# Kernel tuning notes

Measured on AMD Instinct MI355X. Metric: run time of the kernel, lower is better.

Reference implementation:

```python
import jax, jax.numpy as jnp
import numpy as np

H = 16  # n_heads
LN_EPS = 1e-5

def _ln(x, g, b):
    m = jnp.mean(x, axis=-1, keepdims=True)
    v = jnp.mean(jnp.square(x - m), axis=-1, keepdims=True)
    return (x - m) * jax.lax.rsqrt(v + LN_EPS) * g + b

def setup_inputs() -> dict:
    key = jax.random.key(0)
    ks = jax.random.split(key, 12)
    Nq, Nk, D = 4096, 4096, 1024
    s = 1.0 / np.sqrt(D)
    return {
        "query": jax.random.normal(ks[0], (Nq, D), jnp.float32),
        "key_": jax.random.normal(ks[1], (Nk, D), jnp.float32),
        "Wq": jax.random.uniform(ks[2], (D, D), jnp.float32, -s, s),
        "bq": jax.random.uniform(ks[3], (D,), jnp.float32, -s, s),
        "Wk": jax.random.uniform(ks[4], (D, D), jnp.float32, -s, s),
        "bk": jax.random.uniform(ks[5], (D,), jnp.float32, -s, s),
        "Wv": jax.random.uniform(ks[6], (D, D), jnp.float32, -s, s),
        "bv": jax.random.uniform(ks[7], (D,), jnp.float32, -s, s),
        "g1": jnp.ones((D,), jnp.float32),
        "b1": jnp.zeros((D,), jnp.float32),
        "Wl": jax.random.uniform(ks[8], (D, D), jnp.float32, -s, s),
        "bl": jax.random.uniform(ks[9], (D,), jnp.float32, -s, s),
        "g2": jnp.ones((D,), jnp.float32),
        "b2": jnp.zeros((D,), jnp.float32),
    }

def reference(query, key_, Wq, bq, Wk, bk, Wv, bv, g1, b1, Wl, bl, g2, b2):
    Nq, D = query.shape
    Nk = key_.shape[0]
    dh = D // H
    scale = 1.0 / jnp.sqrt(jnp.asarray(D, query.dtype))  # NOTE: full dim_V, not per-head
    Q = (query @ Wq + bq).reshape(Nq, H, dh)   # [Nq,H,dh]
    K = (key_ @ Wk + bk).reshape(Nk, H, dh)    # [Nk,H,dh]
    V = (key_ @ Wv + bv).reshape(Nk, H, dh)    # [Nk,H,dh]
    A = jax.nn.softmax(jnp.einsum('qhd,khd->hqk', Q, K) * scale, axis=-1)  # [H,Nq,Nk]
    O = Q + jnp.einsum('hqk,khd->qhd', A, V)   # residual on projected Q
    out = _ln(O.reshape(Nq, D), g1, b1)
    out = out + jax.nn.relu(out @ Wl + bl)
    return _ln(out, g2, b2)
```

## Files before the change

kernel.cpp:

```cpp
#include <hip/hip_runtime.h>
#include <hip/hip_bf16.h>
#include <stdint.h>

typedef __attribute__((ext_vector_type(4))) float  f32x4;
typedef __attribute__((ext_vector_type(8))) short  bf16x8;
typedef __attribute__((ext_vector_type(4))) float  float4v;
typedef __attribute__((ext_vector_type(4))) unsigned short u16x4;
typedef __attribute__((ext_vector_type(4))) uint32_t u32x4;

typedef uint32_t u32_as1 __attribute__((address_space(1)));
typedef uint32_t u32_as3 __attribute__((address_space(3)));

#define CEXP_SCALE 0.045084221f
#define INV_CEXP   22.180710f

__device__ __forceinline__ void gload_lds16(const void* g, void* l) {
  __builtin_amdgcn_global_load_lds((const u32_as1*)g, (u32_as3*)l, 16, 0, 0);
}

__device__ __forceinline__ unsigned short f2bf(float f) {
  union { float f; uint32_t u; } v; v.f = f;
  uint32_t r = v.u + 0x7fffu + ((v.u >> 16) & 1u);
  return (unsigned short)(r >> 16);
}
__device__ __forceinline__ float bf2f(unsigned short u) {
  union { uint32_t u; float f; } v; v.u = ((uint32_t)u) << 16;
  return v.f;
}
__device__ __forceinline__ uint32_t cvtpk_bf16(float lo, float hi) {
  uint32_t d;
  asm("v_cvt_pk_bf16_f32 %0, %1, %2" : "=v"(d) : "v"(lo), "v"(hi));
  return d;
}
__device__ __forceinline__ float exp2_hw(float x) {
  float r;
  asm("v_exp_f32 %0, %1" : "=v"(r) : "v"(x));
  return r;
}

__global__ __launch_bounds__(256) void wtrans4(const float* __restrict__ W0,
                                               const float* __restrict__ W1,
                                               const float* __restrict__ W2,
                                               const float* __restrict__ W3,
                                               unsigned short* __restrict__ WT, int D) {
  __shared__ float tile[32][33];
  const float* W = (blockIdx.z == 0) ? W0 : (blockIdx.z == 1) ? W1 : (blockIdx.z == 2) ? W2 : W3;
  unsigned short* WTz = WT + (size_t)blockIdx.z * D * D;
  int r0 = blockIdx.x * 32;
  int c0 = blockIdx.y * 32;
  int tc = threadIdx.x & 31;
  int tr = (threadIdx.x >> 5) * 4;
#pragma unroll
  for (int i = 0; i < 4; i++)
    tile[tr + i][tc] = W[(size_t)(r0 + tr + i) * D + c0 + tc];
  __syncthreads();
#pragma unroll
  for (int i = 0; i < 4; i++)
    WTz[(size_t)(c0 + tr + i) * D + r0 + tc] = f2bf(tile[tc][tr + i]);
}

template <int AF32>
__device__ __forceinline__ void gemm_core(
    const void* __restrict__ Ain, const unsigned short* __restrict__ BT,
    const float* __restrict__ bias, const float* __restrict__ bias2,
    unsigned short* __restrict__ C, unsigned short* __restrict__ VtOut,
    const unsigned short* __restrict__ RES,
    int M, int K, int relu_res, float cscale, int bm, int bn,
    unsigned char* AsmRaw, unsigned short* Bsm) {
  int tid = threadIdx.x;
  int lane = tid & 63;
  int w = tid >> 6;
  int wr = (w >> 1) * 64;
  int wc = (w & 1) * 64;
  int r = lane & 15;
  int q4 = lane >> 4;

  f32x4 acc[4][4] = {};

  for (int k0 = 0; k0 < K; k0 += 64) {
    if (AF32) {
      const float* Af = (const float*)Ain;
#pragma unroll
      for (int i = 0; i < 8; i++) {
        int idx = i * 256 + tid;
        int row = idx >> 4;
        int cg = (idx & 15) ^ (row & 15);
        gload_lds16(Af + (size_t)(bm + row) * K + k0 + cg * 4,
                    (float*)AsmRaw + idx * 4);
      }
    } else {
      const unsigned short* Ab = (const unsigned short*)Ain;
#pragma unroll
      for (int i = 0; i < 4; i++) {
        int idx = i * 256 + tid;
        int row = idx >> 3;
        int g = ((idx & 7) ^ (row & 7)) * 8;
        gload_lds16(Ab + (size_t)(bm + row) * K + k0 + g,
                    (unsigned short*)AsmRaw + idx * 8);
      }
    }
#pragma unroll
    for (int i = 0; i < 4; i++) {
      int idx = i * 256 + tid;
      int row = idx >> 3;
      int g = ((idx & 7) ^ (row & 7)) * 8;
      gload_lds16(BT + (size_t)(bn + row) * K + k0 + g, &Bsm[idx * 8]);
    }
    __syncthreads();
#pragma unroll
    for (int kk = 0; kk < 2; kk++) {
      bf16x8 af[4], bfr[4];
      if (AF32) {
        const float* AsF = (const float*)AsmRaw;
        int c0 = kk * 8 + q4 * 2;
#pragma unroll
        for (int mb = 0; mb < 4; mb++) {
          int row = wr + mb * 16 + r;
          const float* rp = AsF + row * 64;
          int x = row & 15;
          f32x4 a0 = *(const f32x4*)(rp + ((c0 ^ x) * 4));
          f32x4 a1 = *(const f32x4*)(rp + (((c0 + 1) ^ x) * 4));
          u32x4 t = {cvtpk_bf16(a0.x, a0.y), cvtpk_bf16(a0.z, a0.w),
                     cvtpk_bf16(a1.x, a1.y), cvtpk_bf16(a1.z, a1.w)};
          af[mb] = __builtin_bit_cast(bf16x8, t);
        }
      } else {
        const unsigned short* AsB = (const unsigned short*)AsmRaw;
        int ch = ((kk * 4 + q4) ^ (r & 7)) * 8;
#pragma unroll
        for (int mb = 0; mb < 4; mb++)
          af[mb] = *(const bf16x8*)&AsB[(wr + mb * 16 + r) * 64 + ch];
      }
      int chb = ((kk * 4 + q4) ^ (r & 7)) * 8;
#pragma unroll
      for (int nb = 0; nb < 4; nb++)
        bfr[nb] = *(const bf16x8*)&Bsm[(wc + nb * 16 + r) * 64 + chb];
#pragma unroll
      for (int mb = 0; mb < 4; mb++)
#pragma unroll
        for (int nb = 0; nb < 4; nb++)
          acc[mb][nb] = __builtin_amdgcn_mfma_f32_16x16x32_bf16(af[mb], bfr[nb], acc[mb][nb], 0, 0, 0);
    }
    __syncthreads();
  }

#pragma unroll
  for (int mb = 0; mb < 4; mb++) {
#pragma unroll
    for (int nb = 0; nb < 4; nb++) {
      int col = bn + wc + nb * 16 + r;
      bool second = (VtOut != nullptr) && (col >= 1024);
      int ccol = second ? (col - 1024) : col;
      float bv = second ? bias2[ccol] : bias[ccol];
      if (second) {
        u16x4 ov;
#pragma unroll
        for (int rr = 0; rr < 4; rr++)
          ov[rr] = f2bf(acc[mb][nb][rr] + bv);
        int row0 = bm + wr + mb * 16 + q4 * 4;
        *(u16x4*)(VtOut + (size_t)ccol * M + row0) = ov;
      } else {
#pragma unroll
        for (int rr = 0; rr < 4; rr++) {
          int row = bm + wr + mb * 16 + q4 * 4 + rr;
          float v = acc[mb][nb][rr] + bv;
          if (relu_res) {
            float res = bf2f(RES[(size_t)row * 1024 + ccol]);
            v = res + (v > 0.f ? v : 0.f);
          }
          C[(size_t)row * 1024 + ccol] = f2bf(v * cscale);
        }
      }
    }
  }
}

__global__ __launch_bounds__(256) void proj_gemm(
    const float* __restrict__ query, const float* __restrict__ key_,
    const unsigned short* __restrict__ WqT, const unsigned short* __restrict__ WkvT,
    const float* __restrict__ bq, const float* __restrict__ bk, const float* __restrict__ bv,
    unsigned short* __restrict__ Qs, unsigned short* __restrict__ Kp,
    unsigned short* __restrict__ Vt, int Nq, int D) {
  __shared__ __align__(16) unsigned char AsmRaw[128 * 64 * 4];
  __shared__ __align__(16) unsigned short Bsm[128 * 64];
  int bid = blockIdx.x;
  if (bid < 256) {
    gemm_core<1>(query, WqT, bq, nullptr, Qs, nullptr, nullptr,
                 Nq, D, 0, CEXP_SCALE, (bid & 31) * 128, (bid >> 5) * 128, AsmRaw, Bsm);
  } else {
    int b = bid - 256;
    gemm_core<1>(key_, WkvT, bk, bv, Kp, Vt, nullptr,
                 Nq, D, 0, 1.0f, (b & 31) * 128, (b >> 5) * 128, AsmRaw, Bsm);
  }
}

__global__ __launch_bounds__(256) void ffn_gemm(
    const unsigned short* __restrict__ A, const unsigned short* __restrict__ WlT,
    const float* __restrict__ bl, unsigned short* __restrict__ C,
    const unsigned short* __restrict__ RES, int Nq, int D) {
  __shared__ __align__(16) unsigned short Asm[2][128 * 64];
  __shared__ __align__(16) unsigned short Bsm[2][128 * 64];
  int tid = threadIdx.x;
  int lane = tid & 63;
  int w = tid >> 6;
  int wr = (w >> 1) * 64;
  int wc = (w & 1) * 64;
  int bid = blockIdx.x;
  int bm = (bid & 31) * 128;
  int bn = (bid >> 5) * 128;
  int r = lane & 15;
  int q4 = lane >> 4;

  f32x4 acc[4][4] = {};

  auto STAGE = [&](int nb, int k0) {
#pragma unroll
    for (int i = 0; i < 4; i++) {
      int idx = i * 256 + tid;
      int row = idx >> 3;
      int g = ((idx & 7) ^ (row & 7)) * 8;
      gload_lds16(A + (size_t)(bm + row) * D + k0 + g, &Asm[nb][idx * 8]);
      gload_lds16(WlT + (size_t)(bn + row) * D + k0 + g, &Bsm[nb][idx * 8]);
    }
  };

  STAGE(0, 0);
  __syncthreads();

  int cur = 0;
  const int NT = D >> 6;
  for (int t = 0; t < NT; ++t) {
    if (t + 1 < NT) STAGE(cur ^ 1, (t + 1) * 64);
#pragma unroll
    for (int kk = 0; kk < 2; kk++) {
      int ch = ((kk * 4 + q4) ^ (r & 7)) * 8;
      bf16x8 af[4], bfr[4];
#pragma unroll
      for (int mb = 0; mb < 4; mb++)
        af[mb] = *(const bf16x8*)&Asm[cur][(wr + mb * 16 + r) * 64 + ch];
#pragma unroll
      for (int nb = 0; nb < 4; nb++)
        bfr[nb] = *(const bf16x8*)&Bsm[cur][(wc + nb * 16 + r) * 64 + ch];
#pragma unroll
      for (int mb = 0; mb < 4; mb++)
#pragma unroll
        for (int nb = 0; nb < 4; nb++)
          acc[mb][nb] = __builtin_amdgcn_mfma_f32_16x16x32_bf16(af[mb], bfr[nb], acc[mb][nb], 0, 0, 0);
    }
    __syncthreads();
    cur ^= 1;
  }

#pragma unroll
  for (int mb = 0; mb < 4; mb++) {
#pragma unroll
    for (int nb = 0; nb < 4; nb++) {
      int col = bn + wc + nb * 16 + r;
      float bv = bl[col];
#pragma unroll
      for (int rr = 0; rr < 4; rr++) {
        int row = bm + wr + mb * 16 + q4 * 4 + rr;
        float v = acc[mb][nb][rr] + bv;
        float res = bf2f(RES[(size_t)row * 1024 + col]);
        v = res + (v > 0.f ? v : 0.f);
        C[(size_t)row * 1024 + col] = f2bf(v);
      }
    }
  }
}

__global__ __launch_bounds__(256, 4) void attn_kernel(
    const unsigned short* __restrict__ Qs,
    const unsigned short* __restrict__ Kp,
    const unsigned short* __restrict__ Vt,
    unsigned short* __restrict__ Opart,
    float* __restrict__ Lpart,
    int Nq, int Nk) {
  __shared__ __align__(16) unsigned short Ksm[2][4096];
  __shared__ __align__(16) unsigned short Vsm[2][4096];
  const int Dm = 1024;
  int tid = threadIdx.x;
  int w = tid >> 6;
  int lane = tid & 63;
  int r = lane & 15;
  int q4 = lane >> 4;
  int bid = blockIdx.x;
  int vid = ((bid & 7) << 7) + (bid >> 3);
  int h = vid >> 6;
  int qw = ((vid >> 1) & 31) * 128 + w * 32;
  int z = vid & 1;
  int k_beg = z * (Nk >> 1);
  const int NT = Nk >> 7;

  const unsigned short* Kb = Kp + h * 64;
  const unsigned short* Vb = Vt + (size_t)h * 64 * Nk;

  int srcA = r + ((lane & 16) << 1);
  int srcB = srcA + 16;
  bool hi_cb = (lane & 32) != 0;

  bf16x8 qf[2][2];
#pragma unroll
  for (int mb = 0; mb < 2; mb++)
#pragma unroll
    for (int s = 0; s < 2; s++)
      qf[mb][s] = *(const bf16x8*)(Qs + (size_t)(qw + mb * 16 + r) * Dm + h * 64 + s * 32 + q4 * 8);

  bf16x8 ones;
#pragma unroll
  for (int i = 0; i < 8; i++) ones[i] = (short)0x3F80;

  const f32x4 czero = {0.f, 0.f, 0.f, 0.f};
  f32x4 acc[2][4] = {};
  f32x4 acc_s[2] = {};

  auto STAGE = [&](int nb, int key0) {
    if (w < 2) {
#pragma unroll
      for (int k = 0; k < 4; k++) {
        int j = w * 4 + k;
        int s = j >> 2, cb = j & 3;
        gload_lds16(Kb + (size_t)(key0 + cb * 16 + r) * Dm + s * 32 + q4 * 8,
                    &Ksm[nb][j * 512]);
      }
    } else {
#pragma unroll
      for (int k = 0; k < 4; k++) {
        int j = (w - 2) * 4 + k;
        int s = j >> 2, db = j & 3;
        gload_lds16(Vb + (size_t)(db * 16 + r) * Nk + key0 + s * 32 + q4 * 8,
                    &Vsm[nb][j * 512]);
      }
    }
  };

  STAGE(0, k_beg);
  __syncthreads();

  int cur = 0;
  for (int t = 0; t < NT; ++t) {
    if (t + 1 < NT) STAGE(cur ^ 1, k_beg + (t + 1) * 64);

    bf16x8 kfr0[4], kfr1[4];
#pragma unroll
    for (int cb = 0; cb < 4; cb++) {
      kfr0[cb] = *(const bf16x8*)&Ksm[cur][(0 * 4 + cb) * 512 + lane * 8];
      kfr1[cb] = *(const bf16x8*)&Ksm[cur][(1 * 4 + cb) * 512 + lane * 8];
    }
    f32x4 sacc[2][4];
#pragma unroll
    for (int cb = 0; cb < 4; cb++)
#pragma unroll
      for (int mb = 0; mb < 2; mb++)
        sacc[mb][cb] = __builtin_amdgcn_mfma_f32_16x16x32_bf16(kfr0[cb], qf[mb][0], czero, 0, 0, 0);
#pragma unroll
    for (int cb = 0; cb < 4; cb++)
#pragma unroll
      for (int mb = 0; mb < 2; mb++)
        sacc[mb][cb] = __builtin_amdgcn_mfma_f32_16x16x32_bf16(kfr1[cb], qf[mb][1], sacc[mb][cb], 0, 0, 0);

    uint32_t pk[2][4][2];
#pragma unroll
    for (int mb = 0; mb < 2; mb++)
#pragma unroll
      for (int cb = 0; cb < 4; cb++) {
        float p0 = exp2_hw(sacc[mb][cb][0]);
        float p1 = exp2_hw(sacc[mb][cb][1]);
        float p2 = exp2_hw(sacc[mb][cb][2]);
        float p3 = exp2_hw(sacc[mb][cb][3]);
        pk[mb][cb][0] = cvtpk_bf16(p0, p1);
        pk[mb][cb][1] = cvtpk_bf16(p2, p3);
      }

#pragma unroll
    for (int s = 0; s < 2; s++) {
      bf16x8 pf[2];
#pragma unroll
      for (int mb = 0; mb < 2; mb++) {
        uint32_t s0 = hi_cb ? pk[mb][2 * s + 1][0] : pk[mb][2 * s][0];
        uint32_t s1 = hi_cb ? pk[mb][2 * s + 1][1] : pk[mb][2 * s][1];
        uint32_t w0 = (uint32_t)__shfl((int)s0, srcA);
        uint32_t w1 = (uint32_t)__shfl((int)s1, srcA);
        uint32_t w2 = (uint32_t)__shfl((int)s0, srcB);
        uint32_t w3 = (uint32_t)__shfl((int)s1, srcB);
        u32x4 tmp = {w0, w1, w2, w3};
        pf[mb] = __builtin_bit_cast(bf16x8, tmp);
      }
      acc_s[0] = __builtin_amdgcn_mfma_f32_16x16x32_bf16(pf[0], ones, acc_s[0], 0, 0, 0);
      acc_s[1] = __builtin_amdgcn_mfma_f32_16x16x32_bf16(pf[1], ones, acc_s[1], 0, 0, 0);
#pragma unroll
      for (int db = 0; db < 4; db++) {
        bf16x8 vfx = *(const bf16x8*)&Vsm[cur][(s * 4 + db) * 512 + lane * 8];
        acc[0][db] = __builtin_amdgcn_mfma_f32_16x16x32_bf16(pf[0], vfx, acc[0][db], 0, 0, 0);
        acc[1][db] = __builtin_amdgcn_mfma_f32_16x16x32_bf16(pf[1], vfx, acc[1][db], 0, 0, 0);
      }
    }

    __syncthreads();
    cur ^= 1;
  }

  unsigned short* Op = Opart + (size_t)z * Nq * Dm;
#pragma unroll
  for (int mb = 0; mb < 2; mb++)
#pragma unroll
    for (int rr = 0; rr < 4; rr++) {
      int qrow = qw + mb * 16 + q4 * 4 + rr;
      if (r == 0)
        Lpart[(size_t)(z * 16 + h) * Nq + qrow] = acc_s[mb][rr];
#pragma unroll
      for (int db = 0; db < 4; db++) {
        int col = h * 64 + db * 16 + r;
        Op[(size_t)qrow * Dm + col] = f2bf(acc[mb][db][rr]);
      }
    }
}

__global__ __launch_bounds__(256) void combine_ln(
    const unsigned short* __restrict__ Qs,
    const unsigned short* __restrict__ Op,
    const float* __restrict__ Lp,
    const float* __restrict__ g, const float* __restrict__ b,
    unsigned short* __restrict__ out, int Nq) {
  int row = blockIdx.x;
  int tid = threadIdx.x;
  int h = tid >> 4;
  size_t base = (size_t)row * 1024 + tid * 4;
  float linv = 1.0f / (Lp[(size_t)h * Nq + row] + Lp[(size_t)(16 + h) * Nq + row]);
  u16x4 qv = *(const u16x4*)(Qs + base);
  u16x4 a0 = *(const u16x4*)(Op + base);
  u16x4 a1 = *(const u16x4*)(Op + (size_t)Nq * 1024 + base);
  float x0 = bf2f(qv.x) * INV_CEXP + (bf2f(a0.x) + bf2f(a1.x)) * linv;
  float x1 = bf2f(qv.y) * INV_CEXP + (bf2f(a0.y) + bf2f(a1.y)) * linv;
  float x2 = bf2f(qv.z) * INV_CEXP + (bf2f(a0.z) + bf2f(a1.z)) * linv;
  float x3 = bf2f(qv.w) * INV_CEXP + (bf2f(a0.w) + bf2f(a1.w)) * linv;
  float s = x0 + x1 + x2 + x3;
  float s2 = x0 * x0 + x1 * x1 + x2 * x2 + x3 * x3;
#pragma unroll
  for (int m = 1; m < 64; m <<= 1) { s += __shfl_xor(s, m); s2 += __shfl_xor(s2, m); }
  __shared__ float red[8];
  int w = tid >> 6, lane = tid & 63;
  if (lane == 0) { red[w] = s; red[4 + w] = s2; }
  __syncthreads();
  s = red[0] + red[1] + red[2] + red[3];
  s2 = red[4] + red[5] + red[6] + red[7];
  float mean = s * (1.0f / 1024.0f);
  float var = s2 * (1.0f / 1024.0f) - mean * mean;
  float inv = rsqrtf(var + 1e-5f);
  float y0 = (x0 - mean) * inv * g[tid * 4 + 0] + b[tid * 4 + 0];
  float y1 = (x1 - mean) * inv * g[tid * 4 + 1] + b[tid * 4 + 1];
  float y2 = (x2 - mean) * inv * g[tid * 4 + 2] + b[tid * 4 + 2];
  float y3 = (x3 - mean) * inv * g[tid * 4 + 3] + b[tid * 4 + 3];
  u16x4 o = {f2bf(y0), f2bf(y1), f2bf(y2), f2bf(y3)};
  *(u16x4*)(out + base) = o;
}

template <int OUTF32>
__global__ __launch_bounds__(256) void ln_kernel(
    const unsigned short* __restrict__ X,
    const float* __restrict__ g, const float* __restrict__ b,
    void* __restrict__ outp, int D) {
  int row = blockIdx.x;
  int tid = threadIdx.x;
  const unsigned short* xr = X + (size_t)row * D;
  u16x4 xv = *(const u16x4*)(xr + tid * 4);
  float x0 = bf2f(xv.x), x1 = bf2f(xv.y), x2 = bf2f(xv.z), x3 = bf2f(xv.w);
  float s = x0 + x1 + x2 + x3;
  float s2 = x0 * x0 + x1 * x1 + x2 * x2 + x3 * x3;
#pragma unroll
  for (int m = 1; m < 64; m <<= 1) { s += __shfl_xor(s, m); s2 += __shfl_xor(s2, m); }
  __shared__ float red[8];
  int w = tid >> 6, lane = tid & 63;
  if (lane == 0) { red[w] = s; red[4 + w] = s2; }
  __syncthreads();
  s = red[0] + red[1] + red[2] + red[3];
  s2 = red[4] + red[5] + red[6] + red[7];
  float mean = s * (1.0f / 1024.0f);
  float var = s2 * (1.0f / 1024.0f) - mean * mean;
  float inv = rsqrtf(var + 1e-5f);
  float y0 = (x0 - mean) * inv * g[tid * 4 + 0] + b[tid * 4 + 0];
  float y1 = (x1 - mean) * inv * g[tid * 4 + 1] + b[tid * 4 + 1];
  float y2 = (x2 - mean) * inv * g[tid * 4 + 2] + b[tid * 4 + 2];
  float y3 = (x3 - mean) * inv * g[tid * 4 + 3] + b[tid * 4 + 3];
  if (OUTF32) {
    float4v o = {y0, y1, y2, y3};
    *(float4v*)((float*)outp + (size_t)row * D + tid * 4) = o;
  } else {
    u16x4 o = {f2bf(y0), f2bf(y1), f2bf(y2), f2bf(y3)};
    *(u16x4*)((unsigned short*)outp + (size_t)row * D + tid * 4) = o;
  }
}

extern "C" void kernel_launch(void* const* d_in, const int* in_sizes, int n_in,
                              void* d_out, int out_size, void* d_ws, size_t ws_size,
                              hipStream_t stream) {
  (void)in_sizes; (void)n_in; (void)out_size; (void)ws_size;
  const float* query = (const float*)d_in[0];
  const float* key_  = (const float*)d_in[1];
  const float* Wq = (const float*)d_in[2];
  const float* bq = (const float*)d_in[3];
  const float* Wk = (const float*)d_in[4];
  const float* bk = (const float*)d_in[5];
  const float* Wv = (const float*)d_in[6];
  const float* bv_ = (const float*)d_in[7];
  const float* g1 = (const float*)d_in[8];
  const float* b1 = (const float*)d_in[9];
  const float* Wl = (const float*)d_in[10];
  const float* bl = (const float*)d_in[11];
  const float* g2 = (const float*)d_in[12];
  const float* b2 = (const float*)d_in[13];
  float* out = (float*)d_out;

  const int Nq = 4096, Nk = 4096, D = 1024;
  const size_t MEl = (size_t)4096 * 1024;
  const size_t DD = (size_t)D * D;

  unsigned short* w16 = (unsigned short*)d_ws;
  unsigned short* WqT = w16;
  unsigned short* WkT = WqT + DD;
  unsigned short* WvT = WkT + DD;
  unsigned short* WlT = WvT + DD;
  unsigned short* Qs  = w16 + 4 * DD;
  unsigned short* Kp  = Qs + MEl;
  unsigned short* Vt  = Kp + MEl;
  unsigned short* Opart = Vt + MEl;
  unsigned short* out1  = Opart + 2 * MEl;
  float* Lpart = (float*)(out1 + MEl);
  unsigned short* out2  = Opart;

  wtrans4<<<dim3(32, 32, 4), 256, 0, stream>>>(Wq, Wk, Wv, Wl, WqT, D);

  proj_gemm<<<768, 256, 0, stream>>>(query, key_, WqT, WkT, bq, bk, bv_,
                                     Qs, Kp, Vt, Nq, D);

  attn_kernel<<<1024, 256, 0, stream>>>(Qs, Kp, Vt, Opart, Lpart, Nq, Nk);

  combine_ln<<<4096, 256, 0, stream>>>(Qs, Opart, Lpart, g1, b1, out1, Nq);
  ffn_gemm<<<256, 256, 0, stream>>>(out1, WlT, bl, out2, out1, Nq, D);
  ln_kernel<1><<<4096, 256, 0, stream>>>(out2, g2, b2, (void*)out, D);
}
```

Measured before the change: 171.6 us.

## Double-buffer projection GEMM, swizzle block order, use permlane swaps in attention

The projection GEMM is rewritten as its own kernel with a BK=32 double-buffered LDS pipeline, so global loads for the next k-tile overlap MFMA work on the current one. Projection and FFN GEMMs now remap block IDs so neighbouring blocks share B tiles, which should help L2 reuse. In the attention kernel, the ds_bpermute shuffles used to rearrange P fragments are replaced by permlane32/permlane16 swap instructions plus selects, cutting LDS traffic. The costs are more loop iterations and barriers per GEMM and extra VALU selects in the attention inner loop.

New measurement: 191.5 us. +11.6%, slower.

```diff
diff --git a/kernel.cpp b/kernel.cpp
--- a/kernel.cpp
+++ b/kernel.cpp
@@ -7,6 +7,7 @@
 typedef __attribute__((ext_vector_type(4))) float  float4v;
 typedef __attribute__((ext_vector_type(4))) unsigned short u16x4;
 typedef __attribute__((ext_vector_type(4))) uint32_t u32x4;
+typedef __attribute__((ext_vector_type(2))) unsigned int uint2v;
 
 typedef uint32_t u32_as1 __attribute__((address_space(1)));
 typedef uint32_t u32_as3 __attribute__((address_space(3)));
@@ -36,6 +37,14 @@
   float r;
   asm("v_exp_f32 %0, %1" : "=v"(r) : "v"(x));
   return r;
+}
+__device__ __forceinline__ void bcast_pair(uint32_t v, bool upper,
+                                           uint32_t& lo, uint32_t& hi) {
+  uint2v p32 = __builtin_amdgcn_permlane32_swap(v, v, false, false);
+  uint32_t s = upper ? p32.y : p32.x;
+  uint2v p16 = __builtin_amdgcn_permlane16_swap(s, s, false, false);
+  lo = p16.x;
+  hi = p16.y;
 }
 
 __global__ __launch_bounds__(256) void wtrans4(const float* __restrict__ W0,
@@ -59,14 +68,14 @@
     WTz[(size_t)(c0 + tr + i) * D + r0 + tc] = f2bf(tile[tc][tr + i]);
 }
 
-template <int AF32>
-__device__ __forceinline__ void gemm_core(
-    const void* __restrict__ Ain, const unsigned short* __restrict__ BT,
-    const float* __restrict__ bias, const float* __restrict__ bias2,
-    unsigned short* __restrict__ C, unsigned short* __restrict__ VtOut,
-    const unsigned short* __restrict__ RES,
-    int M, int K, int relu_res, float cscale, int bm, int bn,
-    unsigned char* AsmRaw, unsigned short* Bsm) {
+__global__ __launch_bounds__(256) void proj_gemm(
+    const float* __restrict__ query, const float* __restrict__ key_,
+    const unsigned short* __restrict__ WqT, const unsigned short* __restrict__ WkvT,
+    const float* __restrict__ bq, const float* __restrict__ bk, const float* __restrict__ bv,
+    unsigned short* __restrict__ Qs, unsigned short* __restrict__ Kp,
+    unsigned short* __restrict__ Vt, int Nq, int D) {
+  __shared__ __align__(16) float         AsmF[2][128 * 32];
+  __shared__ __align__(16) unsigned short Bsm[2][128 * 32];
   int tid = threadIdx.x;
   int lane = tid & 63;
   int w = tid >> 6;
@@ -75,122 +84,102 @@
   int r = lane & 15;
   int q4 = lane >> 4;
 
+  int bid = blockIdx.x;
+  bool isQ = bid < 256;
+  const float* Af;
+  const unsigned short* BT;
+  int bm, bn;
+  if (isQ) {
+    int vid = ((bid & 7) << 5) | (bid >> 3);
+    bm = (vid & 31) * 128; bn = (vid >> 5) * 128;
+    Af = query; BT = WqT;
+  } else {
+    int b = bid - 256;
+    int vid = ((b & 7) << 6) | (b >> 3);
+    bm = (vid & 31) * 128; bn = (vid >> 5) * 128;
+    Af = key_; BT = WkvT;
+  }
+
   f32x4 acc[4][4] = {};
 
-  for (int k0 = 0; k0 < K; k0 += 64) {
-    if (AF32) {
-      const float* Af = (const float*)Ain;
-#pragma unroll
-      for (int i = 0; i < 8; i++) {
-        int idx = i * 256 + tid;
-        int row = idx >> 4;
-        int cg = (idx & 15) ^ (row & 15);
-        gload_lds16(Af + (size_t)(bm + row) * K + k0 + cg * 4,
-                    (float*)AsmRaw + idx * 4);
-      }
-    } else {
-      const unsigned short* Ab = (const unsigned short*)Ain;
-#pragma unroll
-      for (int i = 0; i < 4; i++) {
-        int idx = i * 256 + tid;
-        int row = idx >> 3;
-        int g = ((idx & 7) ^ (row & 7)) * 8;
-        gload_lds16(Ab + (size_t)(bm + row) * K + k0 + g,
-                    (unsigned short*)AsmRaw + idx * 8);
-      }
-    }
+  auto STAGE = [&](int nb, int k0) {
 #pragma unroll
     for (int i = 0; i < 4; i++) {
       int idx = i * 256 + tid;
       int row = idx >> 3;
-      int g = ((idx & 7) ^ (row & 7)) * 8;
-      gload_lds16(BT + (size_t)(bn + row) * K + k0 + g, &Bsm[idx * 8]);
-    }
+      int cg = (idx & 7) ^ (row & 7);
+      gload_lds16(Af + (size_t)(bm + row) * 1024 + k0 + cg * 4, &AsmF[nb][idx * 4]);
+    }
+#pragma unroll
+    for (int i = 0; i < 2; i++) {
+      int idx = i * 256 + tid;
+      int row = idx >> 2;
+      int cg = (idx & 3) ^ (row & 3);
+      gload_lds16(BT + (size_t)(bn + row) * 1024 + k0 + cg * 8, &Bsm[nb][idx * 8]);
+    }
+  };
+
+  STAGE(0, 0);
+  __syncthreads();
+
+  int cur = 0;
+  for (int t = 0; t < 32; ++t) {
+    if (t + 1 < 32) STAGE(cur ^ 1, (t + 1) * 32);
+    bf16x8 af[4], bfr[4];
+    int c0 = q4 * 2;
+    int x = r & 7;
+#pragma unroll
+    for (int mb = 0; mb < 4; mb++) {
+      const float* rp = &AsmF[cur][(wr + mb * 16 + r) * 32];
+      f32x4 a0 = *(const f32x4*)(rp + ((c0 ^ x) * 4));
+      f32x4 a1 = *(const f32x4*)(rp + (((c0 + 1) ^ x) * 4));
+      u32x4 tt = {cvtpk_bf16(a0.x, a0.y), cvtpk_bf16(a0.z, a0.w),
+                  cvtpk_bf16(a1.x, a1.y), cvtpk_bf16(a1.z, a1.w)};
+      af[mb] = __builtin_bit_cast(bf16x8, tt);
+    }
+    int chb = (q4 ^ (r & 3)) * 8;
+#pragma unroll
+    for (int nb = 0; nb < 4; nb++)
+      bfr[nb] = *(const bf16x8*)&Bsm[cur][(wc + nb * 16 + r) * 32 + chb];
+#pragma unroll
+    for (int mb = 0; mb < 4; mb++)
+#pragma unroll
+      for (int nb = 0; nb < 4; nb++)
+        acc[mb][nb] = __builtin_amdgcn_mfma_f32_16x16x32_bf16(af[mb], bfr[nb], acc[mb][nb], 0, 0, 0);
     __syncthreads();
-#pragma unroll
-    for (int kk = 0; kk < 2; kk++) {
-      bf16x8 af[4], bfr[4];
-      if (AF32) {
-        const float* AsF = (const float*)AsmRaw;
-        int c0 = kk * 8 + q4 * 2;
-#pragma unroll
-        for (int mb = 0; mb < 4; mb++) {
-          int row = wr + mb * 16 + r;
-          const float* rp = AsF + row * 64;
-          int x = row & 15;
-          f32x4 a0 = *(const f32x4*)(rp + ((c0 ^ x) * 4));
-          f32x4 a1 = *(const f32x4*)(rp + (((c0 + 1) ^ x) * 4));
-          u32x4 t = {cvtpk_bf16(a0.x, a0.y), cvtpk_bf16(a0.z, a0.w),
-                     cvtpk_bf16(a1.x, a1.y), cvtpk_bf16(a1.z, a1.w)};
-          af[mb] = __builtin_bit_cast(bf16x8, t);
+    cur ^= 1;
+  }
+
+#pragma unroll
+  for (int mb = 0; mb < 4; mb++) {
+#pragma unroll
+    for (int nb = 0; nb < 4; nb++) {
+      int col = bn + wc + nb * 16 + r;
+      if (isQ) {
+        float bv2 = bq[col];
+#pragma unroll
+        for (int rr = 0; rr < 4; rr++) {
+          int row = bm + wr + mb * 16 + q4 * 4 + rr;
+          Qs[(size_t)row * 1024 + col] = f2bf((acc[mb][nb][rr] + bv2) * CEXP_SCALE);
+        }
+      } else if (col < 1024) {
+        float bv2 = bk[col];
+#pragma unroll
+        for (int rr = 0; rr < 4; rr++) {
+          int row = bm + wr + mb * 16 + q4 * 4 + rr;
+          Kp[(size_t)row * 1024 + col] = f2bf(acc[mb][nb][rr] + bv2);
         }
       } else {
-        const unsigned short* AsB = (const unsigned short*)AsmRaw;
-        int ch = ((kk * 4 + q4) ^ (r & 7)) * 8;
-#pragma unroll
-        for (int mb = 0; mb < 4; mb++)
-          af[mb] = *(const bf16x8*)&AsB[(wr + mb * 16 + r) * 64 + ch];
-      }
-      int chb = ((kk * 4 + q4) ^ (r & 7)) * 8;
-#pragma unroll
-      for (int nb = 0; nb < 4; nb++)
-        bfr[nb] = *(const bf16x8*)&Bsm[(wc + nb * 16 + r) * 64 + chb];
-#pragma unroll
-      for (int mb = 0; mb < 4; mb++)
-#pragma unroll
-        for (int nb = 0; nb < 4; nb++)
-          acc[mb][nb] = __builtin_amdgcn_mfma_f32_16x16x32_bf16(af[mb], bfr[nb], acc[mb][nb], 0, 0, 0);
-    }
-    __syncthreads();
-  }
-
-#pragma unroll
-  for (int mb = 0; mb < 4; mb++) {
-#pragma unroll
-    for (int nb = 0; nb < 4; nb++) {
-      int col = bn + wc + nb * 16 + r;
-      bool second = (VtOut != nullptr) && (col >= 1024);
-      int ccol = second ? (col - 1024) : col;
-      float bv = second ? bias2[ccol] : bias[ccol];
-      if (second) {
+        int ccol = col - 1024;
+        float bv2 = bv[ccol];
         u16x4 ov;
 #pragma unroll
         for (int rr = 0; rr < 4; rr++)
-          ov[rr] = f2bf(acc[mb][nb][rr] + bv);
+          ov[rr] = f2bf(acc[mb][nb][rr] + bv2);
         int row0 = bm + wr + mb * 16 + q4 * 4;
-        *(u16x4*)(VtOut + (size_t)ccol * M + row0) = ov;
-      } else {
-#pragma unroll
-        for (int rr = 0; rr < 4; rr++) {
-          int row = bm + wr + mb * 16 + q4 * 4 + rr;
-          float v = acc[mb][nb][rr] + bv;
-          if (relu_res) {
-            float res = bf2f(RES[(size_t)row * 1024 + ccol]);
-            v = res + (v > 0.f ? v : 0.f);
-          }
-          C[(size_t)row * 1024 + ccol] = f2bf(v * cscale);
-        }
-      }
-    }
-  }
-}
-
-__global__ __launch_bounds__(256) void proj_gemm(
-    const float* __restrict__ query, const float* __restrict__ key_,
-    const unsigned short* __restrict__ WqT, const unsigned short* __restrict__ WkvT,
-    const float* __restrict__ bq, const float* __restrict__ bk, const float* __restrict__ bv,
-    unsigned short* __restrict__ Qs, unsigned short* __restrict__ Kp,
-    unsigned short* __restrict__ Vt, int Nq, int D) {
-  __shared__ __align__(16) unsigned char AsmRaw[128 * 64 * 4];
-  __shared__ __align__(16) unsigned short Bsm[128 * 64];
-  int bid = blockIdx.x;
-  if (bid < 256) {
-    gemm_core<1>(query, WqT, bq, nullptr, Qs, nullptr, nullptr,
-                 Nq, D, 0, CEXP_SCALE, (bid & 31) * 128, (bid >> 5) * 128, AsmRaw, Bsm);
-  } else {
-    int b = bid - 256;
-    gemm_core<1>(key_, WkvT, bk, bv, Kp, Vt, nullptr,
-                 Nq, D, 0, 1.0f, (b & 31) * 128, (b >> 5) * 128, AsmRaw, Bsm);
+        *(u16x4*)(Vt + (size_t)ccol * Nq + row0) = ov;
+      }
+    }
   }
 }
 
@@ -206,8 +195,9 @@
   int wr = (w >> 1) * 64;
   int wc = (w & 1) * 64;
   int bid = blockIdx.x;
-  int bm = (bid & 31) * 128;
-  int bn = (bid >> 5) * 128;
+  int vid = ((bid & 7) << 5) | (bid >> 3);
+  int bm = (vid & 31) * 128;
+  int bn = (vid >> 5) * 128;
   int r = lane & 15;
   int q4 = lane >> 4;
 
@@ -295,9 +285,7 @@
   const unsigned short* Kb = Kp + h * 64;
   const unsigned short* Vb = Vt + (size_t)h * 64 * Nk;
 
-  int srcA = r + ((lane & 16) << 1);
-  int srcB = srcA + 16;
-  bool hi_cb = (lane & 32) != 0;
+  bool hi4 = (lane & 16) != 0;
 
   bf16x8 qf[2][2];
 #pragma unroll
@@ -377,12 +365,15 @@
       bf16x8 pf[2];
 #pragma unroll
       for (int mb = 0; mb < 2; mb++) {
-        uint32_t s0 = hi_cb ? pk[mb][2 * s + 1][0] : pk[mb][2 * s][0];
-        uint32_t s1 = hi_cb ? pk[mb][2 * s + 1][1] : pk[mb][2 * s][1];
-        uint32_t w0 = (uint32_t)__shfl((int)s0, srcA);
-        uint32_t w1 = (uint32_t)__shfl((int)s1, srcA);
-        uint32_t w2 = (uint32_t)__shfl((int)s0, srcB);
-        uint32_t w3 = (uint32_t)__shfl((int)s1, srcB);
+        uint32_t ax0, bx0, ax1, bx1, ay0, by0, ay1, by1;
+        bcast_pair(pk[mb][2 * s][0],     false, ax0, bx0);
+        bcast_pair(pk[mb][2 * s][1],     false, ax1, bx1);
+        bcast_pair(pk[mb][2 * s + 1][0], true,  ay0, by0);
+        bcast_pair(pk[mb][2 * s + 1][1], true,  ay1, by1);
+        uint32_t w0 = hi4 ? ay0 : ax0;
+        uint32_t w1 = hi4 ? ay1 : ax1;
+        uint32_t w2 = hi4 ? by0 : bx0;
+        uint32_t w3 = hi4 ? by1 : bx1;
         u32x4 tmp = {w0, w1, w2, w3};
         pf[mb] = __builtin_bit_cast(bf16x8, tmp);
       }
```
